# Optimization experiments

Measured on AMD Instinct MI355X. Metric: run time of the kernel, lower is better.

## Reference

```python
import jax, jax.numpy as jnp
import numpy as np

# Module config (matches init_kwargs)
BATCH = 64
IN_CHANNELS, IN_H, IN_W = 64, 64, 64
OUT_CHANNELS = 256
KH, KW = 2, 2
SH, SW = 1, 1
DH, DW = 1, 1
# effective kernel size with dilation 1 is (2, 2); padding mode 'full' ->
# pad = (kaw-1, kaw-1, kah-1, kah-1) in torch F.pad order (left, right, top, bottom)
PAD_L, PAD_R, PAD_T, PAD_B = 1, 1, 1, 1
SEED = 42  # rand_state = np.random.RandomState(42)


def _make_weight():
    """Replicates the 0/1 selection-mask weight from SpatialProductLayer.__init__."""
    rs = np.random.RandomState(SEED)
    kernels_idx = []
    for _ in range(KH * KW):
        idx = np.arange(OUT_CHANNELS) % IN_CHANNELS
        rs.shuffle(idx)
        kernels_idx.append(idx)
    kernels_idx = np.stack(kernels_idx, axis=1)                       # (O, KH*KW)
    kernels_idx = kernels_idx.reshape(OUT_CHANNELS, 1, KH, KW)        # (O, 1, KH, KW)
    chan = np.arange(IN_CHANNELS).reshape(1, IN_CHANNELS, 1, 1)       # (1, I, 1, 1)
    weight = np.equal(chan, kernels_idx).astype(np.float32)           # (O, I, KH, KW), one-hot over I
    return jnp.asarray(weight)


def setup_inputs() -> dict:
    key = jax.random.key(0)
    x = jax.random.normal(key, (BATCH, IN_CHANNELS, IN_H, IN_W), dtype=jnp.float32)
    return {"x": x, "weight": _make_weight()}


def reference(x, weight):
    # x: (B, C, H, W). Pad exactly like torch.nn.functional.pad(x, (l, r, t, b)).
    xp = jnp.pad(x, ((0, 0), (0, 0), (PAD_T, PAD_B), (PAD_L, PAD_R)))
    # conv2d with stride/dilation; weight is the sparse 0/1 selection mask.
    out = jax.lax.conv_general_dilated(
        xp, weight,
        window_strides=(SH, SW),
        padding='VALID',
        rhs_dilation=(DH, DW),
        dimension_numbers=('NCHW', 'OIHW', 'NCHW'),
    )
    return out  # (B, 256, 65, 65)
```

## Files before the change

### kernel.cpp

```cpp
#include <hip/hip_runtime.h>

#define BATCH 64
#define IC    64
#define IH    64
#define IW    64
#define OC    256
#define OH    65
#define OW    65
#define NTAP  4
#define LROW  (IW + 2)

__global__ void build_idx_kernel(const float* __restrict__ w,
                                 int* __restrict__ idx) {
    int t = blockIdx.x * blockDim.x + threadIdx.x;
    if (t >= OC * NTAP) return;
    int o = t >> 2;
    int p = t & 3;
    const float* wo = w + o * (IC * NTAP) + p;
    int found = 0;
    for (int i = 0; i < IC; ++i) {
        if (wo[i * NTAP] > 0.5f) found = i;
    }
    idx[t] = found;
}

__global__ __launch_bounds__(256) void spl_kernel(
        const float* __restrict__ x,
        const int*   __restrict__ idx_g,
        float*       __restrict__ out) {
    __shared__ float lds[2][IC][LROW];
    __shared__ int   idx_s[OC * NTAP];

    const int y   = blockIdx.x;
    const int b   = blockIdx.y;
    const int tid = threadIdx.x;

    for (int i = tid; i < OC * NTAP; i += 256) idx_s[i] = idx_g[i];

    for (int e = tid; e < 2 * IC * LROW; e += 256) {
        int r    = e / (IC * LROW);
        int rem  = e - r * (IC * LROW);
        int c    = rem / LROW;
        int col  = rem - c * LROW;
        int inrow = y + r - 1;
        int incol = col - 1;
        float v = 0.0f;
        if ((unsigned)inrow < (unsigned)IH && (unsigned)incol < (unsigned)IW)
            v = x[((b * IC + c) * IH + inrow) * IW + incol];
        lds[r][c][col] = v;
    }
    __syncthreads();

    for (int i = tid; i < OC * OW; i += 256) {
        int o  = i / OW;
        int xx = i - o * OW;
        const int* ip = &idx_s[o * NTAP];
        float s = lds[0][ip[0]][xx]     + lds[0][ip[1]][xx + 1]
                + lds[1][ip[2]][xx]     + lds[1][ip[3]][xx + 1];
        out[(((size_t)b * OC + o) * OH + y) * OW + xx] = s;
    }
}

extern "C" void kernel_launch(void* const* d_in, const int* in_sizes, int n_in,
                              void* d_out, int out_size, void* d_ws, size_t ws_size,
                              hipStream_t stream) {
    const float* x = (const float*)d_in[0];
    const float* w = (const float*)d_in[1];
    float* out     = (float*)d_out;
    int*   idx     = (int*)d_ws;

    build_idx_kernel<<<(OC * NTAP + 255) / 256, 256, 0, stream>>>(w, idx);

    dim3 grid(OH, BATCH);
    spl_kernel<<<grid, 256, 0, stream>>>(x, idx, out);
}
```

Measured before the change: 447.8 us.

## Map one block per output plane and gather directly from global memory

Blocks now cover one (output channel, batch) plane instead of one output row, so each block writes a contiguous 65x65 plane. Inputs are read straight from global memory (relying on L2 for reuse) rather than staged through LDS, and the per-channel tap indices are decoded inside the kernel, which removes the separate index-building launch. This cuts per-block staging of all 64 channels and a kernel launch, at the cost of more global reads that depend on cache hits.

```diff
diff --git a/kernel.cpp b/kernel.cpp
--- a/kernel.cpp
+++ b/kernel.cpp
@@ -8,56 +8,56 @@
 #define OH    65
 #define OW    65
 #define NTAP  4
-#define LROW  (IW + 2)
-
-__global__ void build_idx_kernel(const float* __restrict__ w,
-                                 int* __restrict__ idx) {
-    int t = blockIdx.x * blockDim.x + threadIdx.x;
-    if (t >= OC * NTAP) return;
-    int o = t >> 2;
-    int p = t & 3;
-    const float* wo = w + o * (IC * NTAP) + p;
-    int found = 0;
-    for (int i = 0; i < IC; ++i) {
-        if (wo[i * NTAP] > 0.5f) found = i;
-    }
-    idx[t] = found;
-}
+#define PLANE (OH * OW)
 
 __global__ __launch_bounds__(256) void spl_kernel(
         const float* __restrict__ x,
-        const int*   __restrict__ idx_g,
+        const float* __restrict__ w,
         float*       __restrict__ out) {
-    __shared__ float lds[2][IC][LROW];
-    __shared__ int   idx_s[OC * NTAP];
+    const int o = blockIdx.x;
+    const int b = blockIdx.y;
+    const int t = threadIdx.x;
 
-    const int y   = blockIdx.x;
-    const int b   = blockIdx.y;
-    const int tid = threadIdx.x;
-
-    for (int i = tid; i < OC * NTAP; i += 256) idx_s[i] = idx_g[i];
-
-    for (int e = tid; e < 2 * IC * LROW; e += 256) {
-        int r    = e / (IC * LROW);
-        int rem  = e - r * (IC * LROW);
-        int c    = rem / LROW;
-        int col  = rem - c * LROW;
-        int inrow = y + r - 1;
-        int incol = col - 1;
-        float v = 0.0f;
-        if ((unsigned)inrow < (unsigned)IH && (unsigned)incol < (unsigned)IW)
-            v = x[((b * IC + c) * IH + inrow) * IW + incol];
-        lds[r][c][col] = v;
-    }
+    __shared__ int idx_s[NTAP];
+    float wv = w[o * (IC * NTAP) + t];
+    if (wv > 0.5f) idx_s[t & 3] = t >> 2;
     __syncthreads();
 
-    for (int i = tid; i < OC * OW; i += 256) {
-        int o  = i / OW;
-        int xx = i - o * OW;
-        const int* ip = &idx_s[o * NTAP];
-        float s = lds[0][ip[0]][xx]     + lds[0][ip[1]][xx + 1]
-                + lds[1][ip[2]][xx]     + lds[1][ip[3]][xx + 1];
-        out[(((size_t)b * OC + o) * OH + y) * OW + xx] = s;
+    const size_t bbase = (size_t)b * IC * (IH * IW);
+    const float* p00 = x + bbase + (size_t)idx_s[0] * (IH * IW);
+    const float* p01 = x + bbase + (size_t)idx_s[1] * (IH * IW);
+    const float* p10 = x + bbase + (size_t)idx_s[2] * (IH * IW);
+    const float* p11 = x + bbase + (size_t)idx_s[3] * (IH * IW);
+    float* po = out + ((size_t)b * OC + o) * PLANE;
+
+    #pragma unroll 4
+    for (int k = 0; k < 16; ++k) {
+        int i = t + k * 256;
+        int y  = (i * 4033) >> 18;
+        int xx = i - y * 65;
+        int off = (y << 6) + xx;
+        bool yl = (y  >= 1), yh = (y  <= 63);
+        bool xl = (xx >= 1), xh = (xx <= 63);
+        float t00 = (yl && xl) ? p00[off - 65] : 0.0f;
+        float t01 = (yl && xh) ? p01[off - 64] : 0.0f;
+        float t10 = (yh && xl) ? p10[off - 1]  : 0.0f;
+        float t11 = (yh && xh) ? p11[off]      : 0.0f;
+        po[i] = (t00 + t01) + (t10 + t11);
+    }
+    {
+        int i = t + 4096;
+        if (i < PLANE) {
+            int y  = (i * 4033) >> 18;
+            int xx = i - y * 65;
+            int off = (y << 6) + xx;
+            bool yl = (y  >= 1), yh = (y  <= 63);
+            bool xl = (xx >= 1), xh = (xx <= 63);
+            float t00 = (yl && xl) ? p00[off - 65] : 0.0f;
+            float t01 = (yl && xh) ? p01[off - 64] : 0.0f;
+            float t10 = (yh && xl) ? p10[off - 1]  : 0.0f;
+            float t11 = (yh && xh) ? p11[off]      : 0.0f;
+            po[i] = (t00 + t01) + (t10 + t11);
+        }
     }
 }
 
@@ -67,10 +67,7 @@
     const float* x = (const float*)d_in[0];
     const float* w = (const float*)d_in[1];
     float* out     = (float*)d_out;
-    int*   idx     = (int*)d_ws;
 
-    build_idx_kernel<<<(OC * NTAP + 255) / 256, 256, 0, stream>>>(w, idx);
-
-    dim3 grid(OH, BATCH);
-    spl_kernel<<<grid, 256, 0, stream>>>(x, idx, out);
+    dim3 grid(OC, BATCH);
+    spl_kernel<<<grid, 256, 0, stream>>>(x, w, out);
 }
```

After: 426.7 us. 1.05x faster.
